# Optimization experiments

Hardware: AMD Instinct MI355X
Metric: run time of the kernel (lower is better)

Reference implementation:

```python
import jax, jax.numpy as jnp
import numpy as np

NUM_MODELS = 64
IN_CHANNELS = 16
HIDDEN = 128
B, H, W = 16, 32, 32


def setup_inputs() -> dict:
    key = jax.random.key(0)
    k1, k2, k3, k4, k5 = jax.random.split(key, 5)
    M, C, Hd = NUM_MODELS, IN_CHANNELS, HIDDEN
    x = jax.random.normal(k1, (B, M * C, H, W), dtype=jnp.float32)
    # grouped 1x1 conv weights: per-group [out_per_group, in_per_group]
    w1 = jax.random.normal(k2, (M, Hd, 9 * C), dtype=jnp.float32) * 0.05
    b1 = jax.random.normal(k3, (M * Hd,), dtype=jnp.float32) * 0.05
    w2 = jax.random.normal(k4, (M, C, Hd), dtype=jnp.float32) * 0.05
    b2 = jax.random.normal(k5, (M * C,), dtype=jnp.float32) * 0.05
    return {"x": x, "w1": w1, "b1": b1, "w2": w2, "b2": b2}


def _perceive(x):
    # x: [B, M*C, H, W] -> [B, 9*M*C, H, W], order: center, then 8 shifts
    b, mc, h, w = x.shape
    padded = jnp.pad(x, ((0, 0), (0, 0), (1, 1), (1, 1)))
    shifts = [x]
    for r in (-1, 0, 1):
        for c in (-1, 0, 1):
            if r == 0 and c == 0:
                continue
            shifts.append(padded[:, :, r + 1:r + 1 + h, c + 1:c + 1 + w])
    return jnp.concatenate(shifts, axis=1)


def reference(x, w1, b1, w2, b2):
    M, C, Hd = NUM_MODELS, IN_CHANNELS, HIDDEN
    b, _, h, w = x.shape
    perception = _perceive(x)  # [B, 9*M*C, H, W]
    # grouped conv slices contiguous channel blocks of size 9*C per group
    per_g = perception.reshape(b, M, 9 * C, h, w)
    hdn = jnp.einsum('bmchw,mdc->bmdhw', per_g, w1) + b1.reshape(1, M, Hd, 1, 1)
    hdn = jax.nn.relu(hdn)
    dx = jnp.einsum('bmdhw,mcd->bmchw', hdn, w2) + b2.reshape(1, M, C, 1, 1)
    return x + dx.reshape(b, M * C, h, w)
```

## Files before the change

kernel.cpp:

```cpp
#include <hip/hip_runtime.h>
#include <hip/hip_bf16.h>


typedef __attribute__((ext_vector_type(8))) short short8;
typedef __attribute__((ext_vector_type(4))) float f32x4;

constexpr int Bn  = 16;
constexpr int Mn  = 64;
constexpr int Cn  = 16;
constexpr int Hd  = 128;
constexpr int K9  = 144;
constexpr int MCn = 1024;
constexpr int NP  = 64;
constexpr int CHUNKS = 18;
constexpr int BUFB = CHUNKS * NP * 16;
constexpr int HT_STRIDE = 272;
constexpr int NT  = 256;
constexpr int TILES = 16;

constexpr size_t XPM_SLABS = 34 * 34;
constexpr size_t XPM_B     = XPM_SLABS * MCn;
constexpr size_t XPM_BYTES = (size_t)Bn * XPM_B * 2;
constexpr size_t W1_ELEMS  = (size_t)Mn * Hd * K9;
constexpr size_t W2_ELEMS  = (size_t)Mn * Cn * Hd;
constexpr size_t WS_NEED   = XPM_BYTES + 2 * (W1_ELEMS + W2_ELEMS);

constexpr int NB_BORDER = Bn * 132;
constexpr int NB_W      = (int)((W1_ELEMS + W2_ELEMS) / 4 / 256);

__device__ __forceinline__ ushort f2bf(float f) {
    return __bfloat16_as_ushort(__float2bfloat16(f));
}
__device__ __forceinline__ float bf2f(ushort u) {
    union { uint i; float f; } v; v.i = (uint)u << 16; return v.f;
}

__global__ __launch_bounds__(256)
void prep_xpm(const float* __restrict__ x, ushort* __restrict__ xpm)
{
    const int bid = blockIdx.x;
    const int b  = bid >> 7;
    const int h  = (bid >> 2) & 31;
    const int ck = bid & 3;
    const int tid = threadIdx.x;

    __shared__ ushort T[256][36];

    const int mc = ck * 256 + tid;
    const float* src = x + (((size_t)b * MCn + mc) * 32 + h) * 32;
    #pragma unroll
    for (int j = 0; j < 8; ++j) {
        const float4 f = *(const float4*)(src + 4 * j);
        uint2 pk;
        pk.x = (uint)f2bf(f.x) | ((uint)f2bf(f.y) << 16);
        pk.y = (uint)f2bf(f.z) | ((uint)f2bf(f.w) << 16);
        *(uint2*)&T[tid][4 * j] = pk;
    }
    __syncthreads();

    ushort* const dstb = xpm + (size_t)b * XPM_B + ((size_t)(h + 1) * 34) * MCn
                       + ck * 256;
    #pragma unroll
    for (int rep = 0; rep < 4; ++rep) {
        const int q8 = tid & 31;
        const int w  = (tid >> 5) + 8 * rep;
        ushort tmp[8];
        #pragma unroll
        for (int k2 = 0; k2 < 8; ++k2) tmp[k2] = T[8 * q8 + k2][w];
        uint4 v;
        v.x = (uint)tmp[0] | ((uint)tmp[1] << 16);
        v.y = (uint)tmp[2] | ((uint)tmp[3] << 16);
        v.z = (uint)tmp[4] | ((uint)tmp[5] << 16);
        v.w = (uint)tmp[6] | ((uint)tmp[7] << 16);
        *(uint4*)(dstb + (size_t)(w + 1) * MCn + 8 * q8) = v;
    }
}

__global__ __launch_bounds__(256)
void prep_aux(const float* __restrict__ w1, const float* __restrict__ w2,
              ushort* __restrict__ w1bf, ushort* __restrict__ w2bf,
              ushort* __restrict__ xpm)
{
    const int bid = blockIdx.x;
    const int tid = threadIdx.x;
    if (bid < NB_BORDER) {
        const int b   = bid / 132;
        const int pos = bid % 132;
        int hh, ww;
        if      (pos < 34)  { hh = 0;              ww = pos;        }
        else if (pos < 68)  { hh = 33;             ww = pos - 34;   }
        else if (pos < 100) { hh = pos - 68 + 1;   ww = 0;          }
        else                { hh = pos - 100 + 1;  ww = 33;         }
        ushort* dst = xpm + (size_t)b * XPM_B + ((size_t)hh * 34 + ww) * MCn
                    + tid * 4;
        *(uint2*)dst = (uint2){0, 0};
    } else {
        const size_t i = ((size_t)(bid - NB_BORDER) * 256 + tid) * 4;
        const float* src; ushort* dst; size_t e;
        if (i < W1_ELEMS) { src = w1; dst = w1bf; e = i; }
        else              { src = w2; dst = w2bf; e = i - W1_ELEMS; }
        const float4 f = *(const float4*)(src + e);
        uint2 pk;
        pk.x = (uint)f2bf(f.x) | ((uint)f2bf(f.y) << 16);
        pk.y = (uint)f2bf(f.z) | ((uint)f2bf(f.w) << 16);
        *(uint2*)(dst + e) = pk;
    }
}

__global__ __launch_bounds__(NT, 4)
void nca_pipe(const ushort* __restrict__ xpm,
              const ushort* __restrict__ w1bf, const float* __restrict__ b1,
              const ushort* __restrict__ w2bf, const float* __restrict__ b2,
              float* __restrict__ out)
{
    __shared__ __align__(16) char U[2 * BUFB];

    const int tid  = threadIdx.x;
    const int lane = tid & 63;
    const int wid  = tid >> 6;
    const int lr   = lane & 15;
    const int lk   = lane >> 4;

    const int bid   = blockIdx.x;
    const int xcd   = bid & 7;
    const int j     = bid >> 3;
    const int m     = j & 63;
    const int sethi = j >> 6;
    const int bb    = sethi * 8 + xcd;

    const ushort* const xpb = xpm + (size_t)bb * XPM_B;

    short8 a1[2][5];
    #pragma unroll
    for (int rt = 0; rt < 2; ++rt) {
        const int row = wid * 32 + rt * 16 + lr;
        const ushort* wr = w1bf + (m * Hd + row) * K9;
        #pragma unroll
        for (int ks = 0; ks < 5; ++ks) {
            const int k0 = ks * 32 + lk * 8;
            a1[rt][ks] = (k0 < K9) ? *(const short8*)(wr + k0)
                                   : (short8){0,0,0,0,0,0,0,0};
        }
    }
    short8 a2[4];
    #pragma unroll
    for (int ks = 0; ks < 4; ++ks)
        a2[ks] = *(const short8*)(w2bf + (m * Cn + lr) * Hd + ks * 32 + lk * 8);

    const unsigned long long TAB = 0xA62918405ull;
    int cb[5];
    #pragma unroll
    for (int i = 0; i < 5; ++i) {
        const int c = wid + 4 * i;
        const int cc = (c < CHUNKS) ? c : 0;
        const int ch = m * K9 + cc * 8;
        const int s  = ch >> 10;
        const int mc = ch & 1023;
        const uint nib = (uint)(TAB >> (4 * s)) & 15u;
        const int dr = (int)(nib & 3u) - 1;
        const int dc = (int)(nib >> 2) - 1;
        cb[i] = ((dr + 1) * 34 + (dc + 1)) * 1024 + mc;
    }
    const int laneoff = ((lane >> 5) * 34 + (lane & 31)) * 1024;

    auto STAGE = [&](int t, char* buf) {
        const ushort* srcb = xpb + (size_t)(t * 2) * 34816 + laneoff;
        #pragma unroll
        for (int i = 0; i < 5; ++i) {
            const int c = wid + 4 * i;
            if (c < CHUNKS) {
                __builtin_amdgcn_global_load_lds(
                    (const __attribute__((address_space(1))) void*)(srcb + cb[i]),
                    (__attribute__((address_space(3))) void*)(buf + c * 1024),
                    16, 0, 0);
            }
        }
    };

    STAGE(0, U);
    asm volatile("s_waitcnt vmcnt(0)" ::: "memory");
    __syncthreads();

    #pragma unroll 1
    for (int t = 0; t < TILES; ++t) {
        char* const A = U + (t & 1) * BUFB;
        char* const B = U + ((t + 1) & 1) * BUFB;
        if (t + 1 < TILES) STAGE(t + 1, B);

        f32x4 acc[2][4];
        #pragma unroll
        for (int i = 0; i < 2; ++i)
            #pragma unroll
            for (int jj = 0; jj < 4; ++jj) acc[i][jj] = (f32x4){0.f, 0.f, 0.f, 0.f};

        #pragma unroll
        for (int ct = 0; ct < 4; ++ct) {
            const char* pb = A + (ct * 16 + lr) * 16;
            short8 bfrag[5];
            #pragma unroll
            for (int ks = 0; ks < 4; ++ks)
                bfrag[ks] = *(const short8*)(pb + (ks * 4 + lk) * 1024);
            bfrag[4] = (short8){0,0,0,0,0,0,0,0};
            if (lk < 2)
                bfrag[4] = *(const short8*)(pb + (16 + lk) * 1024);
            #pragma unroll
            for (int ks = 0; ks < 5; ++ks) {
                acc[0][ct] = __builtin_amdgcn_mfma_f32_16x16x32_bf16(a1[0][ks], bfrag[ks], acc[0][ct], 0, 0, 0);
                acc[1][ct] = __builtin_amdgcn_mfma_f32_16x16x32_bf16(a1[1][ks], bfrag[ks], acc[1][ct], 0, 0, 0);
            }
        }
        __syncthreads();

        #pragma unroll
        for (int rt = 0; rt < 2; ++rt) {
            const int hd0 = wid * 32 + rt * 16 + lk * 4;
            const float4 bs = *(const float4*)(b1 + m * Hd + hd0);
            #pragma unroll
            for (int ct = 0; ct < 4; ++ct) {
                const int p = ct * 16 + lr;
                const f32x4 v = acc[rt][ct];
                uint2 pk;
                pk.x = (uint)f2bf(fmaxf(v[0] + bs.x, 0.f)) |
                       ((uint)f2bf(fmaxf(v[1] + bs.y, 0.f)) << 16);
                pk.y = (uint)f2bf(fmaxf(v[2] + bs.z, 0.f)) |
                       ((uint)f2bf(fmaxf(v[3] + bs.w, 0.f)) << 16);
                *(uint2*)(A + p * HT_STRIDE + hd0 * 2) = pk;
            }
        }
        __syncthreads();

        f32x4 acc2;
        {
            const char* base = A + (wid * 16 + lr) * HT_STRIDE + lk * 16;
            short8 bbf[4];
            #pragma unroll
            for (int ks = 0; ks < 4; ++ks)
                bbf[ks] = *(const short8*)(base + ks * 64);
            f32x4 a = (f32x4){0.f, 0.f, 0.f, 0.f};
            #pragma unroll
            for (int ks = 0; ks < 4; ++ks)
                a = __builtin_amdgcn_mfma_f32_16x16x32_bf16(a2[ks], bbf[ks], a, 0, 0, 0);
            acc2 = a;
        }
        __syncthreads();

        const int p0 = t * NP;
        {
            const float4 b2v = *(const float4*)(b2 + m * Cn + lk * 4);
            float (*dxT)[NP + 4] = (float(*)[NP + 4])A;
            const float bsv[4] = {b2v.x, b2v.y, b2v.z, b2v.w};
            const int px = wid * 16 + lr;
            const int gp = p0 + px;
            const int h  = gp >> 5, w = gp & 31;
            const ushort* res = xpb + ((h + 1) * 34 + (w + 1)) * MCn + m * Cn + lk * 4;
            #pragma unroll
            for (int rr2 = 0; rr2 < 4; ++rr2)
                dxT[lk * 4 + rr2][px] = acc2[rr2] + bsv[rr2] + bf2f(res[rr2]);
        }
        __syncthreads();
        {
            float (*dxT)[NP + 4] = (float(*)[NP + 4])A;
            const int c = tid >> 4, iq = tid & 15;
            const int px0 = 4 * iq;
            const float4 d0 = *(const float4*)&dxT[c][px0];
            const size_t idx = ((size_t)(bb * MCn + m * Cn + c)) * 1024 + p0 + px0;
            *(float4*)(out + idx) = d0;
        }

        asm volatile("s_waitcnt vmcnt(0)" ::: "memory");
        __syncthreads();
    }
}

constexpr int PT_STRIDE_FB = 304;
__global__ __launch_bounds__(NT, 4)
void nca_mfma_f32src(const float* __restrict__ x,  const float* __restrict__ w1,
                     const float* __restrict__ b1, const float* __restrict__ w2,
                     const float* __restrict__ b2, float* __restrict__ out)
{
    __shared__ __align__(16) char U[128 * PT_STRIDE_FB + 16];
    char* const PtL = U;
    char* const HtL = U;

    const int tid  = threadIdx.x;
    const int lane = tid & 63;
    const int wid  = tid >> 6;
    const int lr   = lane & 15;
    const int lk   = lane >> 4;

    const int bid = blockIdx.x;
    const int xcd = bid & 7;
    const int jb  = bid >> 3;
    const int m   = jb & 63;
    const int g   = (jb >> 6) * 8 + xcd;
    const int b   = g >> 3;
    const int p0  = (g & 7) * 128;

    if (tid <= 128) {
        char* z = PtL + tid * PT_STRIDE_FB + (tid < 128 ? 288 : 0);
        *(int4*)z = (int4){0, 0, 0, 0};
    }

    short8 a1[2][5];
    #pragma unroll
    for (int rt = 0; rt < 2; ++rt) {
        const int row = wid * 32 + rt * 16 + lr;
        const float* wr = w1 + (m * Hd + row) * K9;
        #pragma unroll
        for (int ks = 0; ks < 5; ++ks) {
            const int k0 = ks * 32 + lk * 8;
            short8 t;
            if (k0 < K9) {
                const float4 f0 = *(const float4*)(wr + k0);
                const float4 f1 = *(const float4*)(wr + k0 + 4);
                t[0] = (short)f2bf(f0.x); t[1] = (short)f2bf(f0.y);
                t[2] = (short)f2bf(f0.z); t[3] = (short)f2bf(f0.w);
                t[4] = (short)f2bf(f1.x); t[5] = (short)f2bf(f1.y);
                t[6] = (short)f2bf(f1.z); t[7] = (short)f2bf(f1.w);
            } else t = (short8){0,0,0,0,0,0,0,0};
            a1[rt][ks] = t;
        }
    }
    short8 a2[4];
    #pragma unroll
    for (int ks = 0; ks < 4; ++ks) {
        const float* wr = w2 + (m * Cn + lr) * Hd + ks * 32 + lk * 8;
        const float4 f0 = *(const float4*)(wr);
        const float4 f1 = *(const float4*)(wr + 4);
        short8 t;
        t[0] = (short)f2bf(f0.x); t[1] = (short)f2bf(f0.y);
        t[2] = (short)f2bf(f0.z); t[3] = (short)f2bf(f0.w);
        t[4] = (short)f2bf(f1.x); t[5] = (short)f2bf(f1.y);
        t[6] = (short)f2bf(f1.z); t[7] = (short)f2bf(f1.w);
        a2[ks] = t;
    }
    {
        const int s     = tid & 7;
        const int kpl   = (tid >> 3) & 7;
        const int r     = tid >> 6;
        const int rbase = (g & 7) * 4 + r;
        const float* xb = x + (size_t)b * (MCn * 1024);
        const unsigned long long TAB = 0xA62918405ull;
        #pragma unroll
        for (int it = 0; it < 9; ++it) {
            const int kp = it * 8 + kpl;
            float4 hv[2];
            #pragma unroll
            for (int half = 0; half < 2; ++half) {
                const int ch = m * K9 + kp * 2 + half;
                const int sh = ch >> 10;
                const int mc = ch & 1023;
                const uint nib = (uint)(TAB >> (4 * sh)) & 15u;
                const int dr = (int)(nib & 3u) - 1;
                const int dc = (int)(nib >> 2) - 1;
                const int row = rbase + dr;
                const int wb  = 4 * s + dc;
                const int wc  = min(max(wb, 0), 28);
                float4 f = {0.f, 0.f, 0.f, 0.f};
                if ((unsigned)row < 32u)
                    f = *(const float4*)(xb + (mc * 32 + row) * 32 + wc);
                if (wb < 0)       { f.w = f.z; f.z = f.y; f.y = f.x; f.x = 0.f; }
                else if (wb > 28) { f.x = f.y; f.y = f.z; f.z = f.w; f.w = 0.f; }
                hv[half] = f;
            }
            char* dst = PtL + (r * 32 + 4 * s) * PT_STRIDE_FB + kp * 4;
            *(uint*)(dst)                    = (uint)f2bf(hv[0].x) | ((uint)f2bf(hv[1].x) << 16);
            *(uint*)(dst + PT_STRIDE_FB)     = (uint)f2bf(hv[0].y) | ((uint)f2bf(hv[1].y) << 16);
            *(uint*)(dst + 2 * PT_STRIDE_FB) = (uint)f2bf(hv[0].z) | ((uint)f2bf(hv[1].z) << 16);
            *(uint*)(dst + 3 * PT_STRIDE_FB) = (uint)f2bf(hv[0].w) | ((uint)f2bf(hv[1].w) << 16);
        }
    }
    __syncthreads();

    f32x4 acc[2][8];
    #pragma unroll
    for (int i = 0; i < 2; ++i)
        #pragma unroll
        for (int jj = 0; jj < 8; ++jj) acc[i][jj] = (f32x4){0.f, 0.f, 0.f, 0.f};
    #pragma unroll
    for (int ct = 0; ct < 8; ++ct) {
        const int p = ct * 16 + lr;
        const char* base = PtL + p * PT_STRIDE_FB + lk * 16;
        short8 bfrag[5];
        #pragma unroll
        for (int ks = 0; ks < 5; ++ks)
            bfrag[ks] = *(const short8*)(base + ks * 64);
        #pragma unroll
        for (int ks = 0; ks < 5; ++ks) {
            acc[0][ct] = __builtin_amdgcn_mfma_f32_16x16x32_bf16(a1[0][ks], bfrag[ks], acc[0][ct], 0, 0, 0);
            acc[1][ct] = __builtin_amdgcn_mfma_f32_16x16x32_bf16(a1[1][ks], bfrag[ks], acc[1][ct], 0, 0, 0);
        }
    }
    __syncthreads();
    #pragma unroll
    for (int rt = 0; rt < 2; ++rt) {
        const int hd0 = wid * 32 + rt * 16 + lk * 4;
        const float4 bs = *(const float4*)(b1 + m * Hd + hd0);
        #pragma unroll
        for (int ct = 0; ct < 8; ++ct) {
            const int p = ct * 16 + lr;
            const f32x4 v = acc[rt][ct];
            uint2 pk;
            pk.x = (uint)f2bf(fmaxf(v[0] + bs.x, 0.f)) |
                   ((uint)f2bf(fmaxf(v[1] + bs.y, 0.f)) << 16);
            pk.y = (uint)f2bf(fmaxf(v[2] + bs.z, 0.f)) |
                   ((uint)f2bf(fmaxf(v[3] + bs.w, 0.f)) << 16);
            *(uint2*)(HtL + p * HT_STRIDE + hd0 * 2) = pk;
        }
    }
    __syncthreads();
    f32x4 acc2[2];
    #pragma unroll
    for (int jj = 0; jj < 2; ++jj) {
        const int ct = wid * 2 + jj;
        const int p  = ct * 16 + lr;
        const char* base = HtL + p * HT_STRIDE + lk * 16;
        short8 bbf[4];
        #pragma unroll
        for (int ks = 0; ks < 4; ++ks)
            bbf[ks] = *(const short8*)(base + ks * 64);
        f32x4 a = (f32x4){0.f, 0.f, 0.f, 0.f};
        #pragma unroll
        for (int ks = 0; ks < 4; ++ks)
            a = __builtin_amdgcn_mfma_f32_16x16x32_bf16(a2[ks], bbf[ks], a, 0, 0, 0);
        acc2[jj] = a;
    }
    const float4 b2v = *(const float4*)(b2 + m * Cn + lk * 4);
    const float bsv[4] = {b2v.x, b2v.y, b2v.z, b2v.w};
    #pragma unroll
    for (int jj = 0; jj < 2; ++jj) {
        const int ct = wid * 2 + jj;
        const int gp = p0 + ct * 16 + lr;
        #pragma unroll
        for (int r = 0; r < 4; ++r) {
            const int c   = lk * 4 + r;
            const size_t idx = ((size_t)(b * MCn + m * Cn + c)) * 1024 + gp;
            out[idx] = x[idx] + acc2[jj][r] + bsv[r];
        }
    }
}

extern "C" void kernel_launch(void* const* d_in, const int* in_sizes, int n_in,
                              void* d_out, int out_size, void* d_ws, size_t ws_size,
                              hipStream_t stream)
{
    const float* x  = (const float*)d_in[0];
    const float* w1 = (const float*)d_in[1];
    const float* b1 = (const float*)d_in[2];
    const float* w2 = (const float*)d_in[3];
    const float* b2 = (const float*)d_in[4];
    float* out = (float*)d_out;

    if (ws_size >= WS_NEED) {
        ushort* xpm  = (ushort*)d_ws;
        ushort* w1bf = (ushort*)((char*)d_ws + XPM_BYTES);
        ushort* w2bf = w1bf + W1_ELEMS;
        prep_xpm<<<Bn * 32 * 4, 256, 0, stream>>>(x, xpm);
        prep_aux<<<NB_BORDER + NB_W, 256, 0, stream>>>(w1, w2, w1bf, w2bf, xpm);
        nca_pipe<<<Mn * Bn, NT, 0, stream>>>(xpm, w1bf, b1, w2bf, b2, out);
    } else {
        nca_mfma_f32src<<<Mn * (Bn * 1024 / 128), NT, 0, stream>>>(x, w1, b1, w2, b2, out);
    }
}
```

Measured before the change: 159.9 us.

## Split pixel tiles across 4x more blocks and write output directly from MFMA

Each block now handles a quarter of the image (4 tiles instead of 16). The grid grows to four times as many blocks, and the block-to-(model, batch, quarter) mapping is remapped across XCDs. The second MFMA swaps its operands so each lane holds 4 consecutive pixels for one channel. That lets the epilogue add the bias and residual and store a float4 straight to global memory, dropping the LDS transpose and two barriers. In exchange, the per-block w1/w2 register preload is amortized over fewer tiles, and the pipeline prologue runs more often.

```diff
diff --git a/kernel.cpp b/kernel.cpp
--- a/kernel.cpp
+++ b/kernel.cpp
@@ -16,7 +16,7 @@
 constexpr int BUFB = CHUNKS * NP * 16;
 constexpr int HT_STRIDE = 272;
 constexpr int NT  = 256;
-constexpr int TILES = 16;
+constexpr int TILES = 4;
 
 constexpr size_t XPM_SLABS = 34 * 34;
 constexpr size_t XPM_B     = XPM_SLABS * MCn;
@@ -121,12 +121,15 @@
     const int lr   = lane & 15;
     const int lk   = lane >> 4;
 
-    const int bid   = blockIdx.x;
-    const int xcd   = bid & 7;
-    const int j     = bid >> 3;
-    const int m     = j & 63;
-    const int sethi = j >> 6;
-    const int bb    = sethi * 8 + xcd;
+    const int bid = blockIdx.x;
+    const int xcd = bid & 7;
+    const int j   = bid >> 3;
+    const int mlo = j & 31;
+    const int bhi = (j >> 5) & 1;
+    const int mch = (j >> 6) & 1;
+    const int q   = j >> 7;
+    const int m   = mch * 32 + mlo;
+    const int bb  = bhi * 8 + xcd;
 
     const ushort* const xpb = xpm + (size_t)bb * XPM_B;
 
@@ -164,7 +167,7 @@
     const int laneoff = ((lane >> 5) * 34 + (lane & 31)) * 1024;
 
     auto STAGE = [&](int t, char* buf) {
-        const ushort* srcb = xpb + (size_t)(t * 2) * 34816 + laneoff;
+        const ushort* srcb = xpb + (size_t)(q * 8 + t * 2) * 34816 + laneoff;
         #pragma unroll
         for (int i = 0; i < 5; ++i) {
             const int c = wid + 4 * i;
@@ -232,39 +235,31 @@
         f32x4 acc2;
         {
             const char* base = A + (wid * 16 + lr) * HT_STRIDE + lk * 16;
-            short8 bbf[4];
+            short8 hf[4];
             #pragma unroll
             for (int ks = 0; ks < 4; ++ks)
-                bbf[ks] = *(const short8*)(base + ks * 64);
+                hf[ks] = *(const short8*)(base + ks * 64);
             f32x4 a = (f32x4){0.f, 0.f, 0.f, 0.f};
             #pragma unroll
             for (int ks = 0; ks < 4; ++ks)
-                a = __builtin_amdgcn_mfma_f32_16x16x32_bf16(a2[ks], bbf[ks], a, 0, 0, 0);
+                a = __builtin_amdgcn_mfma_f32_16x16x32_bf16(hf[ks], a2[ks], a, 0, 0, 0);
             acc2 = a;
         }
-        __syncthreads();
-
-        const int p0 = t * NP;
+
         {
-            const float4 b2v = *(const float4*)(b2 + m * Cn + lk * 4);
-            float (*dxT)[NP + 4] = (float(*)[NP + 4])A;
-            const float bsv[4] = {b2v.x, b2v.y, b2v.z, b2v.w};
-            const int px = wid * 16 + lr;
-            const int gp = p0 + px;
-            const int h  = gp >> 5, w = gp & 31;
-            const ushort* res = xpb + ((h + 1) * 34 + (w + 1)) * MCn + m * Cn + lk * 4;
-            #pragma unroll
-            for (int rr2 = 0; rr2 < 4; ++rr2)
-                dxT[lk * 4 + rr2][px] = acc2[rr2] + bsv[rr2] + bf2f(res[rr2]);
-        }
-        __syncthreads();
-        {
-            float (*dxT)[NP + 4] = (float(*)[NP + 4])A;
-            const int c = tid >> 4, iq = tid & 15;
-            const int px0 = 4 * iq;
-            const float4 d0 = *(const float4*)&dxT[c][px0];
-            const size_t idx = ((size_t)(bb * MCn + m * Cn + c)) * 1024 + p0 + px0;
-            *(float4*)(out + idx) = d0;
+            const int p0  = q * 256 + t * NP;
+            const int c   = lr;
+            const int gp0 = p0 + wid * 16 + lk * 4;
+            const int h   = gp0 >> 5, w0 = gp0 & 31;
+            const float bsv = b2[m * Cn + c];
+            const ushort* res = xpb + ((h + 1) * 34 + (w0 + 1)) * MCn + m * Cn + c;
+            float4 o;
+            o.x = acc2[0] + bsv + bf2f(res[0]);
+            o.y = acc2[1] + bsv + bf2f(res[MCn]);
+            o.z = acc2[2] + bsv + bf2f(res[2 * MCn]);
+            o.w = acc2[3] + bsv + bf2f(res[3 * MCn]);
+            const size_t idx = ((size_t)(bb * MCn + m * Cn + c)) * 1024 + gp0;
+            *(float4*)(out + idx) = o;
         }
 
         asm volatile("s_waitcnt vmcnt(0)" ::: "memory");
@@ -457,7 +452,7 @@
         ushort* w2bf = w1bf + W1_ELEMS;
         prep_xpm<<<Bn * 32 * 4, 256, 0, stream>>>(x, xpm);
         prep_aux<<<NB_BORDER + NB_W, 256, 0, stream>>>(w1, w2, w1bf, w2bf, xpm);
-        nca_pipe<<<Mn * Bn, NT, 0, stream>>>(xpm, w1bf, b1, w2bf, b2, out);
+        nca_pipe<<<Mn * Bn * TILES, NT, 0, stream>>>(xpm, w1bf, b1, w2bf, b2, out);
     } else {
         nca_mfma_f32src<<<Mn * (Bn * 1024 / 128), NT, 0, stream>>>(x, w1, b1, w2, b2, out);
     }
```

After: 155.7 us. 1.03x faster.
